# Optimization experiments

Measured on AMD Instinct MI355X. Metric: run time of the kernel, lower is better.

Reference implementation:

```python
import jax, jax.numpy as jnp
import numpy as np

BN_EPS = 1e-5


def setup_inputs() -> dict:
    key = jax.random.key(0)
    k1, k2 = jax.random.split(key)
    B, C, H, W = 8, 2048, 64, 64
    x = jax.random.normal(k1, (B, C, H, W), dtype=jnp.float32)
    # grouped Conv1d(channel, channel, k=3, groups=channel, bias=False) weight, squeezed to [C,3]
    cfc_w = jax.random.normal(k2, (C, 3), dtype=jnp.float32) * 0.1
    bn_w = jnp.ones((C,), dtype=jnp.float32)
    bn_b = jnp.zeros((C,), dtype=jnp.float32)
    return {"x": x, "cfc_w": cfc_w, "bn_w": bn_w, "bn_b": bn_b}


def reference(x, cfc_w, bn_w, bn_b):
    b, c, h, w = x.shape
    xf = x.reshape(b, c, h * w)
    mean = jnp.mean(xf, axis=-1)                 # [b,c]  (AdaptiveAvgPool2d(1))
    mx = jnp.max(xf, axis=-1)                    # [b,c]  (AdaptiveMaxPool2d(1))
    std = jnp.std(xf, axis=-1, ddof=1)           # [b,c]  torch unbiased std
    u = jnp.stack([mean, mx, std], axis=-1)      # [b,c,3]
    # MS: per-batch median over all c*3 entries, cubed centering (detached in torch)
    med = jnp.median(u.reshape(b, -1), axis=-1)[:, None, None]
    u = jax.lax.stop_gradient((u - med) ** 3)    # [b,c,3]
    # grouped conv1d, kernel 3, no padding -> output length 1
    z = jnp.einsum('bck,ck->bc', u, cfc_w)       # [b,c]
    # BatchNorm1d eval: running_mean=0, running_var=1
    z = z / jnp.sqrt(jnp.float32(1.0) + BN_EPS) * bn_w + bn_b
    g = jax.nn.sigmoid(z)                        # [b,c]
    return x * g[:, :, None, None]
```

## Files before the change

kernel.cpp:

```cpp
#include <hip/hip_runtime.h>
#include <math.h>

#define HW    4096
#define C_CH  2048
#define B_N   8
#define BN_EPS 1e-5f

__global__ __launch_bounds__(256) void stats_kernel(const float* __restrict__ x,
                                                    float* __restrict__ u) {
    const int bc = blockIdx.x;
    const float4* xb = (const float4*)(x + (size_t)bc * HW);
    const int t = threadIdx.x;

    double sum = 0.0, sumsq = 0.0;
    float mx = -INFINITY;
#pragma unroll
    for (int i = 0; i < 4; ++i) {
        float4 v = xb[t + i * 256];
        sum   += (double)v.x + (double)v.y + (double)v.z + (double)v.w;
        sumsq += (double)v.x * v.x + (double)v.y * v.y +
                 (double)v.z * v.z + (double)v.w * v.w;
        mx = fmaxf(mx, fmaxf(fmaxf(v.x, v.y), fmaxf(v.z, v.w)));
    }

#pragma unroll
    for (int off = 32; off > 0; off >>= 1) {
        sum   += __shfl_down(sum, off);
        sumsq += __shfl_down(sumsq, off);
        mx = fmaxf(mx, __shfl_down(mx, off));
    }

    __shared__ double s_sum[4], s_sq[4];
    __shared__ float  s_mx[4];
    const int wave = t >> 6;
    if ((t & 63) == 0) { s_sum[wave] = sum; s_sq[wave] = sumsq; s_mx[wave] = mx; }
    __syncthreads();

    if (t == 0) {
        double S = 0.0, Q = 0.0; float M = -INFINITY;
#pragma unroll
        for (int w = 0; w < 4; ++w) { S += s_sum[w]; Q += s_sq[w]; M = fmaxf(M, s_mx[w]); }
        double mean = S / (double)HW;
        double var  = (Q - S * S / (double)HW) / (double)(HW - 1);
        if (var < 0.0) var = 0.0;
        u[bc * 3 + 0] = (float)mean;
        u[bc * 3 + 1] = M;
        u[bc * 3 + 2] = (float)sqrt(var);
    }
}

__global__ __launch_bounds__(1024) void gate_kernel(const float* __restrict__ u,
                                                    const float* __restrict__ cfc_w,
                                                    const float* __restrict__ bn_w,
                                                    const float* __restrict__ bn_b,
                                                    float* __restrict__ g) {
    __shared__ float s[8192];
    const int b = blockIdx.x, t = threadIdx.x;
    const float* ub = u + (size_t)b * (C_CH * 3);

    for (int i = t; i < 8192; i += 1024)
        s[i] = (i < C_CH * 3) ? ub[i] : INFINITY;

    for (int k = 2; k <= 8192; k <<= 1) {
        for (int j = k >> 1; j > 0; j >>= 1) {
            __syncthreads();
            for (int i = t; i < 8192; i += 1024) {
                const int ixj = i ^ j;
                if (ixj > i) {
                    float a = s[i], c = s[ixj];
                    const bool dir = ((i & k) == 0);
                    if ((a > c) == dir) { s[i] = c; s[ixj] = a; }
                }
            }
        }
    }
    __syncthreads();

    const float med = 0.5f * (s[3071] + s[3072]);
    const float inv = rsqrtf(1.0f + BN_EPS);

    for (int c = t; c < C_CH; c += 1024) {
        float d0 = ub[c * 3 + 0] - med;
        float d1 = ub[c * 3 + 1] - med;
        float d2 = ub[c * 3 + 2] - med;
        float z = d0 * d0 * d0 * cfc_w[c * 3 + 0] +
                  d1 * d1 * d1 * cfc_w[c * 3 + 1] +
                  d2 * d2 * d2 * cfc_w[c * 3 + 2];
        z = z * inv * bn_w[c] + bn_b[c];
        g[b * C_CH + c] = 1.0f / (1.0f + expf(-z));
    }
}

__global__ __launch_bounds__(256) void apply_kernel(const float* __restrict__ x,
                                                    const float* __restrict__ g,
                                                    float* __restrict__ out) {
    const size_t v = (size_t)blockIdx.x * 256 + threadIdx.x;
    const float gg = g[v >> 10];
    float4 xv = ((const float4*)x)[v];
    float4 o;
    o.x = xv.x * gg; o.y = xv.y * gg; o.z = xv.z * gg; o.w = xv.w * gg;
    ((float4*)out)[v] = o;
}

extern "C" void kernel_launch(void* const* d_in, const int* in_sizes, int n_in,
                              void* d_out, int out_size, void* d_ws, size_t ws_size,
                              hipStream_t stream) {
    const float* x     = (const float*)d_in[0];
    const float* cfc_w = (const float*)d_in[1];
    const float* bn_w  = (const float*)d_in[2];
    const float* bn_b  = (const float*)d_in[3];
    float* out = (float*)d_out;

    float* u = (float*)d_ws;
    float* g = u + (size_t)B_N * C_CH * 3;

    stats_kernel<<<B_N * C_CH, 256, 0, stream>>>(x, u);
    gate_kernel<<<B_N, 1024, 0, stream>>>(u, cfc_w, bn_w, bn_b, g);

    const int total_f4 = (B_N * C_CH * HW) / 4;
    apply_kernel<<<total_f4 / 256, 256, 0, stream>>>(x, g, out);
}
```

Baseline: 572.4 us.

## Use radix-select median, wave-per-row stats, and nontemporal stores in apply

The stats kernel now gives each 64-lane wave one (b,c) row, which removes the shared-memory block reduction and the __syncthreads. The gate kernel replaces the 8192-element bitonic sort with a histogram-based radix select over order-preserving uint keys, run twice to find the two middle ranks. The apply kernel writes its output with nontemporal vector stores to reduce cache pollution. The radix select uses shared atomics and a serial scan on thread 0, and the stats kernel now runs fewer blocks with more loads per thread.

```diff
diff --git a/kernel.cpp b/kernel.cpp
--- a/kernel.cpp
+++ b/kernel.cpp
@@ -6,17 +6,20 @@
 #define B_N   8
 #define BN_EPS 1e-5f
 
+typedef float f32x4 __attribute__((ext_vector_type(4)));
+
 __global__ __launch_bounds__(256) void stats_kernel(const float* __restrict__ x,
                                                     float* __restrict__ u) {
-    const int bc = blockIdx.x;
+    const int wave = threadIdx.x >> 6;
+    const int lane = threadIdx.x & 63;
+    const int bc   = blockIdx.x * 4 + wave;
     const float4* xb = (const float4*)(x + (size_t)bc * HW);
-    const int t = threadIdx.x;
 
     double sum = 0.0, sumsq = 0.0;
     float mx = -INFINITY;
 #pragma unroll
-    for (int i = 0; i < 4; ++i) {
-        float4 v = xb[t + i * 256];
+    for (int i = 0; i < 16; ++i) {
+        float4 v = xb[lane + i * 64];
         sum   += (double)v.x + (double)v.y + (double)v.z + (double)v.w;
         sumsq += (double)v.x * v.x + (double)v.y * v.y +
                  (double)v.z * v.z + (double)v.w * v.w;
@@ -30,56 +33,75 @@
         mx = fmaxf(mx, __shfl_down(mx, off));
     }
 
-    __shared__ double s_sum[4], s_sq[4];
-    __shared__ float  s_mx[4];
-    const int wave = t >> 6;
-    if ((t & 63) == 0) { s_sum[wave] = sum; s_sq[wave] = sumsq; s_mx[wave] = mx; }
-    __syncthreads();
-
-    if (t == 0) {
-        double S = 0.0, Q = 0.0; float M = -INFINITY;
-#pragma unroll
-        for (int w = 0; w < 4; ++w) { S += s_sum[w]; Q += s_sq[w]; M = fmaxf(M, s_mx[w]); }
-        double mean = S / (double)HW;
-        double var  = (Q - S * S / (double)HW) / (double)(HW - 1);
+    if (lane == 0) {
+        double mean = sum / (double)HW;
+        double var  = (sumsq - sum * sum / (double)HW) / (double)(HW - 1);
         if (var < 0.0) var = 0.0;
         u[bc * 3 + 0] = (float)mean;
-        u[bc * 3 + 1] = M;
+        u[bc * 3 + 1] = mx;
         u[bc * 3 + 2] = (float)sqrt(var);
     }
 }
 
-__global__ __launch_bounds__(1024) void gate_kernel(const float* __restrict__ u,
-                                                    const float* __restrict__ cfc_w,
-                                                    const float* __restrict__ bn_w,
-                                                    const float* __restrict__ bn_b,
-                                                    float* __restrict__ g) {
-    __shared__ float s[8192];
+__global__ __launch_bounds__(256) void gate_kernel(const float* __restrict__ u,
+                                                   const float* __restrict__ cfc_w,
+                                                   const float* __restrict__ bn_w,
+                                                   const float* __restrict__ bn_b,
+                                                   float* __restrict__ g) {
+    __shared__ unsigned int keys[C_CH * 3];
+    __shared__ unsigned int hist[256];
+    __shared__ unsigned int s_prefix, s_rank;
+
     const int b = blockIdx.x, t = threadIdx.x;
     const float* ub = u + (size_t)b * (C_CH * 3);
 
-    for (int i = t; i < 8192; i += 1024)
-        s[i] = (i < C_CH * 3) ? ub[i] : INFINITY;
-
-    for (int k = 2; k <= 8192; k <<= 1) {
-        for (int j = k >> 1; j > 0; j >>= 1) {
-            __syncthreads();
-            for (int i = t; i < 8192; i += 1024) {
-                const int ixj = i ^ j;
-                if (ixj > i) {
-                    float a = s[i], c = s[ixj];
-                    const bool dir = ((i & k) == 0);
-                    if ((a > c) == dir) { s[i] = c; s[ixj] = a; }
-                }
-            }
-        }
+    for (int i = t; i < C_CH * 3; i += 256) {
+        unsigned int k = __float_as_uint(ub[i]);
+        keys[i] = (k & 0x80000000u) ? ~k : (k | 0x80000000u);
     }
     __syncthreads();
 
-    const float med = 0.5f * (s[3071] + s[3072]);
+    float med_vals[2];
+#pragma unroll
+    for (int which = 0; which < 2; ++which) {
+        unsigned int prefix = 0;
+        unsigned int rank   = 3071u + (unsigned)which;
+        for (int shift = 24; shift >= 0; shift -= 8) {
+            hist[t] = 0;
+            __syncthreads();
+            const unsigned int mask =
+                (shift == 24) ? 0u : (0xFFFFFFFFu << (shift + 8));
+            for (int i = t; i < C_CH * 3; i += 256) {
+                const unsigned int k = keys[i];
+                if ((k & mask) == prefix)
+                    atomicAdd(&hist[(k >> shift) & 255u], 1u);
+            }
+            __syncthreads();
+            if (t == 0) {
+                unsigned int cum = 0;
+                for (int bin = 0; bin < 256; ++bin) {
+                    const unsigned int c = hist[bin];
+                    if (rank < cum + c) {
+                        s_prefix = prefix | ((unsigned int)bin << shift);
+                        s_rank   = rank - cum;
+                        break;
+                    }
+                    cum += c;
+                }
+            }
+            __syncthreads();
+            prefix = s_prefix;
+            rank   = s_rank;
+        }
+        const unsigned int k = prefix;
+        med_vals[which] =
+            __uint_as_float((k & 0x80000000u) ? (k ^ 0x80000000u) : ~k);
+    }
+
+    const float med = 0.5f * (med_vals[0] + med_vals[1]);
     const float inv = rsqrtf(1.0f + BN_EPS);
 
-    for (int c = t; c < C_CH; c += 1024) {
+    for (int c = t; c < C_CH; c += 256) {
         float d0 = ub[c * 3 + 0] - med;
         float d1 = ub[c * 3 + 1] - med;
         float d2 = ub[c * 3 + 2] - med;
@@ -96,10 +118,9 @@
                                                     float* __restrict__ out) {
     const size_t v = (size_t)blockIdx.x * 256 + threadIdx.x;
     const float gg = g[v >> 10];
-    float4 xv = ((const float4*)x)[v];
-    float4 o;
-    o.x = xv.x * gg; o.y = xv.y * gg; o.z = xv.z * gg; o.w = xv.w * gg;
-    ((float4*)out)[v] = o;
+    const f32x4 xv = ((const f32x4*)x)[v];
+    const f32x4 o  = xv * gg;
+    __builtin_nontemporal_store(o, &((f32x4*)out)[v]);
 }
 
 extern "C" void kernel_launch(void* const* d_in, const int* in_sizes, int n_in,
@@ -114,8 +135,8 @@
     float* u = (float*)d_ws;
     float* g = u + (size_t)B_N * C_CH * 3;
 
-    stats_kernel<<<B_N * C_CH, 256, 0, stream>>>(x, u);
-    gate_kernel<<<B_N, 1024, 0, stream>>>(u, cfc_w, bn_w, bn_b, g);
+    stats_kernel<<<(B_N * C_CH) / 4, 256, 0, stream>>>(x, u);
+    gate_kernel<<<B_N, 256, 0, stream>>>(u, cfc_w, bn_w, bn_b, g);
 
     const int total_f4 = (B_N * C_CH * HW) / 4;
     apply_kernel<<<total_f4 / 256, 256, 0, stream>>>(x, g, out);
```

Measured after the change: 587.8 us. 2.7% more time.
